# Kernel tuning notes

Measured on AMD Instinct MI355X. Metric: run time of the kernel, lower is better.

The kernel has to match this reference:

```python
import jax, jax.numpy as jnp
import numpy as np
import math

T, B, I, H = 512, 64, 256, 512


def setup_inputs() -> dict:
    key = jax.random.key(0)
    ks = jax.random.split(key, 8)
    inp = {}
    inp["x"] = jax.random.normal(ks[0], (T, B, I), jnp.float32)
    # positive elapsed-time intervals per step/batch
    inp["time"] = jax.random.uniform(ks[1], (T, B), jnp.float32, 0.0, 2.0)
    def wn(k, shape, fan_in):
        return jax.random.normal(k, shape, jnp.float32) * (1.0 / math.sqrt(fan_in))
    # forward-direction cell params
    inp["W_ih_f"] = wn(ks[2], (I, 4 * H), I)
    inp["W_hh_f"] = wn(ks[3], (H, 4 * H), H)
    inp["b_f"] = jnp.zeros((4 * H,), jnp.float32)
    inp["W_d_f"] = wn(ks[4], (H, H), H)
    inp["b_d_f"] = jnp.zeros((H,), jnp.float32)
    # backward-direction cell params
    inp["W_ih_b"] = wn(ks[5], (I, 4 * H), I)
    inp["W_hh_b"] = wn(ks[6], (H, 4 * H), H)
    inp["b_b"] = jnp.zeros((4 * H,), jnp.float32)
    inp["W_d_b"] = wn(ks[7], (H, H), H)
    inp["b_d_b"] = jnp.zeros((H,), jnp.float32)
    return inp


def _run_direction(x, t, W_ih, W_hh, b, W_d, b_d):
    """Time-aware LSTM scan over leading axis. x: [T,B,I], t: [T,B]."""
    Bz = x.shape[1]
    Hh = W_hh.shape[0]
    E = jnp.float32(math.e)

    def step(carry, xt_tt):
        h, c = carry
        xt, tt = xt_tt  # [B,I], [B]
        # TLSTM-style time decay of short-term memory
        c_s = jnp.tanh(c @ W_d + b_d)                 # [B,H]
        c_s_hat = c_s / jnp.log(E + tt[:, None])      # decayed short-term
        c_adj = c - c_s + c_s_hat                     # adjusted cell memory
        gates = xt @ W_ih + h @ W_hh + b              # [B,4H]
        i, f, g, o = jnp.split(gates, 4, axis=-1)
        i = jax.nn.sigmoid(i)
        f = jax.nn.sigmoid(f)
        o = jax.nn.sigmoid(o)
        c_new = f * c_adj + i * jnp.tanh(g)
        h_new = o * jnp.tanh(c_new)
        return (h_new, c_new), h_new

    init = (jnp.zeros((Bz, Hh), x.dtype), jnp.zeros((Bz, Hh), x.dtype))
    _, ys = jax.lax.scan(step, init, (x, t))
    return ys  # [T,B,H]


def reference(x, time, W_ih_f, W_hh_f, b_f, W_d_f, b_d_f,
              W_ih_b, W_hh_b, b_b, W_d_b, b_d_b):
    out_f = _run_direction(x, time, W_ih_f, W_hh_f, b_f, W_d_f, b_d_f)
    # reverse direction: flip time axis, scan, flip outputs back
    out_b = _run_direction(x[::-1], time[::-1], W_ih_b, W_hh_b, b_b, W_d_b, b_d_b)[::-1]
    return jnp.concatenate([out_f, out_b], axis=-1)  # [T,B,2H]
```

## Files before the change

kernel.cpp:

```cpp
#include <hip/hip_runtime.h>
#include <cstdint>

#define T_DIM 512
#define B_DIM 64
#define I_DIM 256
#define H_DIM 512

typedef _Float16 f16x8 __attribute__((ext_vector_type(8)));
typedef float f32x4  __attribute__((ext_vector_type(4)));
typedef unsigned int u32x4 __attribute__((ext_vector_type(4)));

union H8U { f16x8 v; u32x4 u; };

#define WS_FLAGS   0u
#define WS_STATE   32768u
#define GRP_U32    16384u
#define WS_XPK     (32768u + 8u*65536u)
#define XPK_U32    (512u*4u*8u*64u*4u)
#define WS_NEED_MIN WS_XPK
#define WS_NEED_XPK (WS_XPK + XPK_U32*4u)

__device__ __forceinline__ unsigned short f2h(float f) {
  union { _Float16 h; unsigned short u; } c; c.h = (_Float16)f; return c.u;
}
__device__ __forceinline__ float sigm(float v) { return 1.0f / (1.0f + __expf(-v)); }
__device__ __forceinline__ float tanh_f(float v) {
  float e = __expf(2.0f * fabsf(v));
  float r = 1.0f - 2.0f / (e + 1.0f);
  return copysignf(r, v);
}

__device__ __forceinline__ void st_u32(unsigned* p, unsigned v) {
  asm volatile("global_store_dword %0, %1, off sc0 sc1" :: "v"(p), "v"(v) : "memory");
}
__device__ __forceinline__ unsigned ld_u32(const unsigned* p) {
  unsigned v;
  asm volatile("global_load_dword %0, %1, off sc0 sc1\n\ts_waitcnt vmcnt(0)"
               : "=v"(v) : "v"(p) : "memory");
  return v;
}

__global__ void __launch_bounds__(256) init_ws_kernel(unsigned* ws) {
  unsigned n = WS_FLAGS + 32768u / 4u;
  for (unsigned i = blockIdx.x * 256u + threadIdx.x; i < n; i += gridDim.x * 256u)
    __hip_atomic_store(&ws[i], 0u, __ATOMIC_RELAXED, __HIP_MEMORY_SCOPE_AGENT);
}

__global__ void __launch_bounds__(256) xpack_kernel(const float* __restrict__ x,
                                                    unsigned* __restrict__ xpk) {
  size_t idx = (size_t)blockIdx.x * 256 + threadIdx.x;
  int l = (int)(idx & 63);
  size_t kt = (idx >> 6) & 7, mt = (idx >> 9) & 3, t = idx >> 11;
  const float* xp = x + ((t * 64) + mt * 16 + (size_t)(l & 15)) * 256 + kt * 32 + (size_t)(l >> 4) * 8;
  f32x4 a = *(const f32x4*)xp, b = *(const f32x4*)(xp + 4);
  float v[8] = {a[0], a[1], a[2], a[3], b[0], b[1], b[2], b[3]};
  u32x4 pk;
  #pragma unroll
  for (int i = 0; i < 4; ++i)
    pk[i] = (unsigned)f2h(v[2 * i]) | ((unsigned)f2h(v[2 * i + 1]) << 16);
  *(u32x4*)(xpk + idx * 4) = pk;
}

template <bool XPK>
__global__ void __launch_bounds__(256, 1) lstm_kernel(
    const float* __restrict__ x, const float* __restrict__ tim,
    const float* __restrict__ Wih_f, const float* __restrict__ Whh_f,
    const float* __restrict__ bias_f, const float* __restrict__ Wd_f,
    const float* __restrict__ bd_f,
    const float* __restrict__ Wih_b, const float* __restrict__ Whh_b,
    const float* __restrict__ bias_b, const float* __restrict__ Wd_b,
    const float* __restrict__ bd_b,
    float* __restrict__ out, char* __restrict__ wsb,
    const unsigned* __restrict__ xpk)
{
  const int tid = threadIdx.x;
  const int w   = tid >> 6;
  const int l   = tid & 63;
  const int lw  = l & 15;
  const int ko  = l >> 4;
  const int g   = blockIdx.x & 7;
  const int js  = blockIdx.x >> 3;
  const int dir = g & 1;
  const int mt  = g >> 1;
  const int b0  = mt * 16;

  const float* Wih  = dir ? Wih_b  : Wih_f;
  const float* Whh  = dir ? Whh_b  : Whh_f;
  const float* bias = dir ? bias_b : bias_f;
  const float* Wd   = dir ? Wd_b   : Wd_f;
  const float* bd   = dir ? bd_b   : bd_f;

  unsigned* flagbase = (unsigned*)(wsb + WS_FLAGS) + (size_t)g * 1024;
  unsigned* state = (unsigned*)(wsb + WS_STATE) + (size_t)g * GRP_U32;

  __shared__ float red[4][5][16][34];

  f16x8 wx[4][2][2];
  f16x8 wh[4][4][2];
  f16x8 wd[4][2];
  #pragma unroll
  for (int xi = 0; xi < 2; ++xi) {
    const int krow = (w * 2 + xi) * 32 + ko * 8;
    #pragma unroll
    for (int g4 = 0; g4 < 4; ++g4) {
      #pragma unroll
      for (int ct = 0; ct < 2; ++ct) {
        const float* p = Wih + (size_t)krow * 2048 + g4 * 512 + js * 32 + ct * 16 + lw;
        #pragma unroll
        for (int i = 0; i < 8; ++i) wx[g4][xi][ct][i] = (_Float16)p[(size_t)i * 2048];
      }
    }
  }
  #pragma unroll
  for (int q = 0; q < 4; ++q) {
    const int krow = w * 128 + q * 32 + ko * 8;
    #pragma unroll
    for (int g4 = 0; g4 < 4; ++g4) {
      #pragma unroll
      for (int ct = 0; ct < 2; ++ct) {
        const float* p = Whh + (size_t)krow * 2048 + g4 * 512 + js * 32 + ct * 16 + lw;
        #pragma unroll
        for (int i = 0; i < 8; ++i) wh[g4][q][ct][i] = (_Float16)p[(size_t)i * 2048];
      }
    }
    #pragma unroll
    for (int ct = 0; ct < 2; ++ct) {
      const float* p2 = Wd + (size_t)krow * 512 + js * 32 + ct * 16 + lw;
      #pragma unroll
      for (int i = 0; i < 8; ++i) wd[q][ct][i] = (_Float16)p2[(size_t)i * 512];
    }
  }

  const int ub = tid >> 4;
  const int uj = tid & 15;
  float bs_i[2], bs_f[2], bs_g[2], bs_o[2], bs_d[2], c_reg[2];
  #pragma unroll
  for (int ct = 0; ct < 2; ++ct) {
    const int jg = js * 32 + ct * 16 + uj;
    bs_i[ct] = bias[jg];
    bs_f[ct] = bias[512 + jg];
    bs_g[ct] = bias[1024 + jg];
    bs_o[ct] = bias[1536 + jg];
    bs_d[ct] = bd[jg];
    c_reg[ct] = 0.0f;
  }

  const unsigned* myflag = flagbase + (size_t)((4 * w + (l >> 2)) * 4 + (l & 3)) * 16;
  unsigned* relflag = flagbase + (size_t)(js * 4 + w) * 16;

  u32x4 rr[4][2];
  u32x4 xpf0, xpf1;

#define ISSUE_KT(kt) do { \
    const unsigned* sp_ = state + (size_t)lslot * 8192 + (size_t)lw * 512 + w * 128 + (kt) * 32 + ko * 8; \
    asm volatile( \
        "global_load_dwordx4 %0, %2, off sc0 sc1\n\t" \
        "global_load_dwordx4 %1, %2, off offset:16 sc0 sc1" \
        : "=&v"(rr[kt][0]), "=&v"(rr[kt][1]) : "v"(sp_) : "memory"); \
  } while (0)

#define MFMA_KT(kt) do { \
    H8U hf_, cf_; \
    hf_.u[0] = __builtin_amdgcn_perm(rr[kt][0][1], rr[kt][0][0], 0x07060302u); \
    hf_.u[1] = __builtin_amdgcn_perm(rr[kt][0][3], rr[kt][0][2], 0x07060302u); \
    hf_.u[2] = __builtin_amdgcn_perm(rr[kt][1][1], rr[kt][1][0], 0x07060302u); \
    hf_.u[3] = __builtin_amdgcn_perm(rr[kt][1][3], rr[kt][1][2], 0x07060302u); \
    cf_.u[0] = __builtin_amdgcn_perm(rr[kt][0][1], rr[kt][0][0], 0x05040100u); \
    cf_.u[1] = __builtin_amdgcn_perm(rr[kt][0][3], rr[kt][0][2], 0x05040100u); \
    cf_.u[2] = __builtin_amdgcn_perm(rr[kt][1][1], rr[kt][1][0], 0x05040100u); \
    cf_.u[3] = __builtin_amdgcn_perm(rr[kt][1][3], rr[kt][1][2], 0x05040100u); \
    _Pragma("unroll") \
    for (int g4 = 0; g4 < 4; ++g4) { \
      _Pragma("unroll") \
      for (int ct = 0; ct < 2; ++ct) \
        ag[g4][ct] = __builtin_amdgcn_mfma_f32_16x16x32_f16(hf_.v, wh[g4][kt][ct], ag[g4][ct], 0, 0, 0); \
    } \
    _Pragma("unroll") \
    for (int ct = 0; ct < 2; ++ct) \
      ac[ct] = __builtin_amdgcn_mfma_f32_16x16x32_f16(cf_.v, wd[kt][ct], ac[ct], 0, 0, 0); \
  } while (0)

  if (XPK) {
    const int ts0 = dir ? (T_DIM - 1) : 0;
    const unsigned* xb = xpk + (((size_t)ts0 * 4 + mt) * 8 + w * 2) * 256 + (size_t)l * 4;
    asm volatile(
        "global_load_dwordx4 %0, %2, off\n\t"
        "global_load_dwordx4 %1, %3, off"
        : "=v"(xpf0), "=v"(xpf1) : "v"(xb), "v"(xb + 256) : "memory");
    asm volatile("s_waitcnt vmcnt(0)" ::: "memory");
    __builtin_amdgcn_sched_barrier(0);
  }

  for (int t = 0; t < T_DIM; ++t) {
    const int tsrc = dir ? (T_DIM - 1 - t) : t;
    const int sslot = t & 1;
    const int lslot = sslot ^ 1;

    float tt = tim[(size_t)tsrc * B_DIM + b0 + ub];

    f16x8 ax[2];
    if (XPK) {
      H8U u0, u1; u0.u = xpf0; u1.u = xpf1;
      ax[0] = u0.v; ax[1] = u1.v;
    } else {
      #pragma unroll
      for (int xi = 0; xi < 2; ++xi) {
        const float* xp = x + ((size_t)tsrc * B_DIM + b0 + lw) * I_DIM + (w * 2 + xi) * 32 + ko * 8;
        f32x4 v0 = *(const f32x4*)xp;
        f32x4 v1 = *(const f32x4*)(xp + 4);
        f16x8 vv;
        #pragma unroll
        for (int i = 0; i < 4; ++i) { vv[i] = (_Float16)v0[i]; vv[4 + i] = (_Float16)v1[i]; }
        ax[xi] = vv;
      }
    }

    f32x4 ag[4][2]; f32x4 ac[2];
    #pragma unroll
    for (int g4 = 0; g4 < 4; ++g4) { ag[g4][0] = (f32x4)0.0f; ag[g4][1] = (f32x4)0.0f; }
    ac[0] = (f32x4)0.0f; ac[1] = (f32x4)0.0f;
    #pragma unroll
    for (int xi = 0; xi < 2; ++xi) {
      #pragma unroll
      for (int g4 = 0; g4 < 4; ++g4) {
        #pragma unroll
        for (int ct = 0; ct < 2; ++ct)
          ag[g4][ct] = __builtin_amdgcn_mfma_f32_16x16x32_f16(ax[xi], wx[g4][xi][ct], ag[g4][ct], 0, 0, 0);
      }
    }

    if (t > 0) {
      if (l < 16) {
        while (ld_u32(myflag) < (unsigned)t) { }
      }
      __builtin_amdgcn_sched_barrier(0);

      ISSUE_KT(0); ISSUE_KT(1); ISSUE_KT(2); ISSUE_KT(3);
      if (XPK) {
        const int tn = (t + 1 < T_DIM) ? (dir ? (T_DIM - 2 - t) : (t + 1)) : 0;
        const unsigned* xbn = xpk + (((size_t)tn * 4 + mt) * 8 + w * 2) * 256 + (size_t)l * 4;
        asm volatile(
            "global_load_dwordx4 %0, %2, off\n\t"
            "global_load_dwordx4 %1, %3, off"
            : "=v"(xpf0), "=v"(xpf1) : "v"(xbn), "v"(xbn + 256) : "memory");
      }

      if (XPK) { asm volatile("s_waitcnt vmcnt(8)" ::: "memory"); }
      else     { asm volatile("s_waitcnt vmcnt(6)" ::: "memory"); }
      __builtin_amdgcn_sched_barrier(0);
      MFMA_KT(0);
      if (XPK) { asm volatile("s_waitcnt vmcnt(6)" ::: "memory"); }
      else     { asm volatile("s_waitcnt vmcnt(4)" ::: "memory"); }
      __builtin_amdgcn_sched_barrier(0);
      MFMA_KT(1);
      if (XPK) { asm volatile("s_waitcnt vmcnt(4)" ::: "memory"); }
      else     { asm volatile("s_waitcnt vmcnt(2)" ::: "memory"); }
      __builtin_amdgcn_sched_barrier(0);
      MFMA_KT(2);
      if (XPK) { asm volatile("s_waitcnt vmcnt(2)" ::: "memory"); }
      else     { asm volatile("s_waitcnt vmcnt(0)" ::: "memory"); }
      __builtin_amdgcn_sched_barrier(0);
      MFMA_KT(3);
    } else if (XPK) {
      const int tn = dir ? (T_DIM - 2) : 1;
      const unsigned* xbn = xpk + (((size_t)tn * 4 + mt) * 8 + w * 2) * 256 + (size_t)l * 4;
      asm volatile(
          "global_load_dwordx4 %0, %2, off\n\t"
          "global_load_dwordx4 %1, %3, off"
          : "=v"(xpf0), "=v"(xpf1) : "v"(xbn), "v"(xbn + 256) : "memory");
    }

    #pragma unroll
    for (int g4 = 0; g4 < 4; ++g4) {
      #pragma unroll
      for (int ct = 0; ct < 2; ++ct) {
        f32x4 s = ag[g4][ct];
        #pragma unroll
        for (int r = 0; r < 4; ++r) red[w][g4][ko * 4 + r][ct * 16 + lw] = s[r];
      }
    }
    #pragma unroll
    for (int ct = 0; ct < 2; ++ct) {
      f32x4 s = ac[ct];
      #pragma unroll
      for (int r = 0; r < 4; ++r) red[w][4][ko * 4 + r][ct * 16 + lw] = s[r];
    }
    asm volatile("s_waitcnt lgkmcnt(0)" ::: "memory");
    __builtin_amdgcn_s_barrier();

    const float dinv = 1.0f / __logf(2.718281828459045f + tt);
    float h_keep[2];
    #pragma unroll
    for (int ct = 0; ct < 2; ++ct) {
      const int cj = ct * 16 + uj;
      float gi = red[0][0][ub][cj] + red[1][0][ub][cj] + red[2][0][ub][cj] + red[3][0][ub][cj] + bs_i[ct];
      float gf = red[0][1][ub][cj] + red[1][1][ub][cj] + red[2][1][ub][cj] + red[3][1][ub][cj] + bs_f[ct];
      float gg = red[0][2][ub][cj] + red[1][2][ub][cj] + red[2][2][ub][cj] + red[3][2][ub][cj] + bs_g[ct];
      float go = red[0][3][ub][cj] + red[1][3][ub][cj] + red[2][3][ub][cj] + red[3][3][ub][cj] + bs_o[ct];
      float csv = red[0][4][ub][cj] + red[1][4][ub][cj] + red[2][4][ub][cj] + red[3][4][ub][cj] + bs_d[ct];

      float c_s = tanh_f(csv);
      float c_adj = c_reg[ct] - c_s + c_s * dinv;
      float iv = sigm(gi);
      float fv = sigm(gf);
      float ov = sigm(go);
      float gv = tanh_f(gg);
      float c_new = fv * c_adj + iv * gv;
      float h_new = ov * tanh_f(c_new);
      c_reg[ct] = c_new;
      h_keep[ct] = h_new;

      const int jglob = js * 32 + cj;
      unsigned val = ((unsigned)f2h(h_new) << 16) | (unsigned)f2h(c_new);
      st_u32(state + (size_t)sslot * 8192 + (size_t)ub * 512 + jglob, val);
    }

    asm volatile("s_waitcnt vmcnt(0)" ::: "memory");
    __builtin_amdgcn_sched_barrier(0);
    if (l == 0) st_u32(relflag, (unsigned)(t + 1));

    #pragma unroll
    for (int ct = 0; ct < 2; ++ct)
      out[((size_t)tsrc * B_DIM + b0 + ub) * 1024 + dir * 512 + js * 32 + ct * 16 + uj] = h_keep[ct];

    __builtin_amdgcn_s_barrier();
  }
#undef ISSUE_KT
#undef MFMA_KT
}

extern "C" void kernel_launch(void* const* d_in, const int* in_sizes, int n_in,
                              void* d_out, int out_size, void* d_ws, size_t ws_size,
                              hipStream_t stream) {
  (void)in_sizes; (void)n_in; (void)out_size;
  if (ws_size < (size_t)WS_NEED_MIN) return;
  const bool use_xpk = ws_size >= (size_t)WS_NEED_XPK;

  const float* x     = (const float*)d_in[0];
  const float* tim   = (const float*)d_in[1];
  const float* Wih_f = (const float*)d_in[2];
  const float* Whh_f = (const float*)d_in[3];
  const float* b_f   = (const float*)d_in[4];
  const float* Wd_f  = (const float*)d_in[5];
  const float* bd_f  = (const float*)d_in[6];
  const float* Wih_b = (const float*)d_in[7];
  const float* Whh_b = (const float*)d_in[8];
  const float* b_b   = (const float*)d_in[9];
  const float* Wd_b  = (const float*)d_in[10];
  const float* bd_b  = (const float*)d_in[11];
  float* out = (float*)d_out;
  char* ws = (char*)d_ws;
  unsigned* xpk = (unsigned*)(ws + WS_XPK);

  hipLaunchKernelGGL(init_ws_kernel, dim3(8), dim3(256), 0, stream, (unsigned*)ws);
  if (use_xpk) {
    hipLaunchKernelGGL(xpack_kernel, dim3(4096), dim3(256), 0, stream, x, xpk);
    hipLaunchKernelGGL((lstm_kernel<true>), dim3(128), dim3(256), 0, stream,
                       x, tim, Wih_f, Whh_f, b_f, Wd_f, bd_f,
                       Wih_b, Whh_b, b_b, Wd_b, bd_b, out, ws, xpk);
  } else {
    hipLaunchKernelGGL((lstm_kernel<false>), dim3(128), dim3(256), 0, stream,
                       x, tim, Wih_f, Whh_f, b_f, Wd_f, bd_f,
                       Wih_b, Whh_b, b_b, Wd_b, bd_b, out, ws, (const unsigned*)nullptr);
  }
}
```

Before: 1.685 ms.

## Tag state words with step parity bits to drop store drain before flag release

Embeds a 3-bit step tag in the low mantissa bits of each packed fp16 cell-state value. Consumers check the tag and reload when it is stale, so the producer no longer waits for its state stores to complete (vmcnt(0)) before publishing the release flag. The state region is pre-initialised with a non-matching tag, and the tag bits are overwritten with a constant before the MFMA, which slightly lowers the precision of c. The LDS reduction padding also changes from 34 to 33. Correctness rests on the tag check together with memory ordering, and stale reads add retry loops.

```diff
diff --git a/kernel.cpp b/kernel.cpp
--- a/kernel.cpp
+++ b/kernel.cpp
@@ -41,9 +41,9 @@
 }
 
 __global__ void __launch_bounds__(256) init_ws_kernel(unsigned* ws) {
-  unsigned n = WS_FLAGS + 32768u / 4u;
+  unsigned n = WS_XPK / 4u;
   for (unsigned i = blockIdx.x * 256u + threadIdx.x; i < n; i += gridDim.x * 256u)
-    __hip_atomic_store(&ws[i], 0u, __ATOMIC_RELAXED, __HIP_MEMORY_SCOPE_AGENT);
+    __hip_atomic_store(&ws[i], (i < 8192u) ? 0u : 5u, __ATOMIC_RELAXED, __HIP_MEMORY_SCOPE_AGENT);
 }
 
 __global__ void __launch_bounds__(256) xpack_kernel(const float* __restrict__ x,
@@ -93,7 +93,7 @@
   unsigned* flagbase = (unsigned*)(wsb + WS_FLAGS) + (size_t)g * 1024;
   unsigned* state = (unsigned*)(wsb + WS_STATE) + (size_t)g * GRP_U32;
 
-  __shared__ float red[4][5][16][34];
+  __shared__ float red[4][5][16][33];
 
   f16x8 wx[4][2][2];
   f16x8 wh[4][4][2];
@@ -159,6 +159,22 @@
         : "=&v"(rr[kt][0]), "=&v"(rr[kt][1]) : "v"(sp_) : "memory"); \
   } while (0)
 
+#define TAGOK(kt) __all((int)( \
+    ((rr[kt][0][0] & 7u) == e3) & ((rr[kt][0][1] & 7u) == e3) & \
+    ((rr[kt][0][2] & 7u) == e3) & ((rr[kt][0][3] & 7u) == e3) & \
+    ((rr[kt][1][0] & 7u) == e3) & ((rr[kt][1][1] & 7u) == e3) & \
+    ((rr[kt][1][2] & 7u) == e3) & ((rr[kt][1][3] & 7u) == e3)))
+
+#define RETRY_KT(kt) do { \
+    if (!TAGOK(kt)) { \
+      do { \
+        ISSUE_KT(kt); \
+        asm volatile("s_waitcnt vmcnt(0)" ::: "memory"); \
+        __builtin_amdgcn_sched_barrier(0); \
+      } while (!TAGOK(kt)); \
+    } \
+  } while (0)
+
 #define MFMA_KT(kt) do { \
     H8U hf_, cf_; \
     hf_.u[0] = __builtin_amdgcn_perm(rr[kt][0][1], rr[kt][0][0], 0x07060302u); \
@@ -170,6 +186,8 @@
     cf_.u[2] = __builtin_amdgcn_perm(rr[kt][1][1], rr[kt][1][0], 0x05040100u); \
     cf_.u[3] = __builtin_amdgcn_perm(rr[kt][1][3], rr[kt][1][2], 0x05040100u); \
     _Pragma("unroll") \
+    for (int j = 0; j < 4; ++j) cf_.u[j] = (cf_.u[j] & 0xFFF8FFF8u) | 0x00040004u; \
+    _Pragma("unroll") \
     for (int g4 = 0; g4 < 4; ++g4) { \
       _Pragma("unroll") \
       for (int ct = 0; ct < 2; ++ct) \
@@ -196,6 +214,11 @@
     const int sslot = t & 1;
     const int lslot = sslot ^ 1;
 
+    if (XPK) {
+      asm volatile("s_waitcnt vmcnt(5)" ::: "memory");
+      __builtin_amdgcn_sched_barrier(0);
+    }
+
     float tt = tim[(size_t)tsrc * B_DIM + b0 + ub];
 
     f16x8 ax[2];
@@ -245,22 +268,24 @@
             : "=v"(xpf0), "=v"(xpf1) : "v"(xbn), "v"(xbn + 256) : "memory");
       }
 
+      const unsigned e3 = (((unsigned)(t - 1)) >> 1) & 7u;
+
       if (XPK) { asm volatile("s_waitcnt vmcnt(8)" ::: "memory"); }
       else     { asm volatile("s_waitcnt vmcnt(6)" ::: "memory"); }
       __builtin_amdgcn_sched_barrier(0);
-      MFMA_KT(0);
+      RETRY_KT(0); MFMA_KT(0);
       if (XPK) { asm volatile("s_waitcnt vmcnt(6)" ::: "memory"); }
       else     { asm volatile("s_waitcnt vmcnt(4)" ::: "memory"); }
       __builtin_amdgcn_sched_barrier(0);
-      MFMA_KT(1);
+      RETRY_KT(1); MFMA_KT(1);
       if (XPK) { asm volatile("s_waitcnt vmcnt(4)" ::: "memory"); }
       else     { asm volatile("s_waitcnt vmcnt(2)" ::: "memory"); }
       __builtin_amdgcn_sched_barrier(0);
-      MFMA_KT(2);
+      RETRY_KT(2); MFMA_KT(2);
       if (XPK) { asm volatile("s_waitcnt vmcnt(2)" ::: "memory"); }
       else     { asm volatile("s_waitcnt vmcnt(0)" ::: "memory"); }
       __builtin_amdgcn_sched_barrier(0);
-      MFMA_KT(3);
+      RETRY_KT(3); MFMA_KT(3);
     } else if (XPK) {
       const int tn = dir ? (T_DIM - 2) : 1;
       const unsigned* xbn = xpk + (((size_t)tn * 4 + mt) * 8 + w * 2) * 256 + (size_t)l * 4;
@@ -289,6 +314,7 @@
     __builtin_amdgcn_s_barrier();
 
     const float dinv = 1.0f / __logf(2.718281828459045f + tt);
+    const unsigned ptag = (((unsigned)t) >> 1) & 7u;
     float h_keep[2];
     #pragma unroll
     for (int ct = 0; ct < 2; ++ct) {
@@ -311,11 +337,11 @@
       h_keep[ct] = h_new;
 
       const int jglob = js * 32 + cj;
-      unsigned val = ((unsigned)f2h(h_new) << 16) | (unsigned)f2h(c_new);
+      unsigned ch = ((unsigned)f2h(c_new) & 0xFFF8u) | ptag;
+      unsigned val = ((unsigned)f2h(h_new) << 16) | ch;
       st_u32(state + (size_t)sslot * 8192 + (size_t)ub * 512 + jglob, val);
     }
 
-    asm volatile("s_waitcnt vmcnt(0)" ::: "memory");
     __builtin_amdgcn_sched_barrier(0);
     if (l == 0) st_u32(relflag, (unsigned)(t + 1));
 
@@ -326,6 +352,8 @@
     __builtin_amdgcn_s_barrier();
   }
 #undef ISSUE_KT
+#undef TAGOK
+#undef RETRY_KT
 #undef MFMA_KT
 }
 
@@ -352,7 +380,7 @@
   char* ws = (char*)d_ws;
   unsigned* xpk = (unsigned*)(ws + WS_XPK);
 
-  hipLaunchKernelGGL(init_ws_kernel, dim3(8), dim3(256), 0, stream, (unsigned*)ws);
+  hipLaunchKernelGGL(init_ws_kernel, dim3(64), dim3(256), 0, stream, (unsigned*)ws);
   if (use_xpk) {
     hipLaunchKernelGGL(xpack_kernel, dim3(4096), dim3(256), 0, stream, x, xpk);
     hipLaunchKernelGGL((lstm_kernel<true>), dim3(128), dim3(256), 0, stream,
```

New measurement: 1.828 ms. 1.08x slower.
